# Optimization experiments

Measured on AMD Instinct MI355X. Metric: run time of the kernel, lower is better.

The kernel has to match this reference:

```python
import jax, jax.numpy as jnp
import numpy as np

HIDDEN_DIM = 128
ATTN_DIM = 64
B, N = 2, 512

def setup_inputs() -> dict:
    key = jax.random.key(0)
    ks = jax.random.split(key, 8)
    s = 0.05
    return {
        "X":    jax.random.normal(ks[0], (B, N, HIDDEN_DIM), dtype=jnp.float32),
        "Wo":   jax.random.normal(ks[1], (ATTN_DIM, HIDDEN_DIM), dtype=jnp.float32) * s,
        "W1":   jax.random.normal(ks[2], (ATTN_DIM, HIDDEN_DIM), dtype=jnp.float32) * s,
        "Wphi": jax.random.normal(ks[3], (ATTN_DIM,), dtype=jnp.float32) * s,
        "Wy":   jax.random.normal(ks[4], (HIDDEN_DIM, HIDDEN_DIM), dtype=jnp.float32) * s,
        "by":   jax.random.normal(ks[5], (HIDDEN_DIM,), dtype=jnp.float32) * s,
        "We":   jax.random.normal(ks[6], (HIDDEN_DIM, ATTN_DIM), dtype=jnp.float32) * s,
        "be":   jax.random.normal(ks[7], (HIDDEN_DIM,), dtype=jnp.float32) * s,
    }

def reference(X, Wo, W1, Wphi, Wy, by, We, be):
    # h_o, h_1: [B, N, A]
    h_o = jnp.einsum('bnc,ac->bna', X, Wo)
    h_1 = jnp.einsum('bnc,ac->bna', X, W1)
    # pairwise tanh edge features e_ij: [B, N, N, A]
    e = jnp.tanh(h_o[:, :, None, :] + h_1[:, None, :, :])
    # scores [B, N, N] via w_phi projection, row-wise softmax over j
    scores = jnp.einsum('bija,a->bij', e, Wphi)
    alpha = jax.nn.softmax(scores, axis=-1)
    # value path 1: Wy x_j -> aggregated by alpha (bmm)
    X_y = jnp.einsum('bnc,hc->bnh', X, Wy) + by
    part1 = jnp.einsum('bij,bjh->bih', alpha, X_y)
    # value path 2: We e_ij -> weighted sum over j
    eval_ = jnp.einsum('bija,ha->bijh', e, We) + be  # [B, N, N, H]
    part2 = jnp.einsum('bij,bijh->bih', alpha, eval_)
    return part1 + part2
```

## Files before the change

kernel.cpp:

```cpp
#include <hip/hip_runtime.h>

#define B_ 2
#define N_ 512
#define C_ 128
#define A_ 64
#define H_ 128
#define TI 2

#define SC2L 2.885390081777927f
#define NEG2LE -2.885390081777927f

#define OFF_WET 0
#define OFF_V   (OFF_WET + A_*H_)
#define OFF_US  (OFF_V  + B_*N_*A_)
#define OFF_UQ  (OFF_US + B_*N_*A_)
#define OFF_XY  (OFF_UQ + B_*N_*A_)

__device__ __forceinline__ float fexp2(float x) { return __builtin_amdgcn_exp2f(x); }
__device__ __forceinline__ float frcp(float x)  { return __builtin_amdgcn_rcpf(x); }

__global__ __launch_bounds__(512) void proj_kernel(
    const float* __restrict__ X, const float* __restrict__ Wo,
    const float* __restrict__ W1, const float* __restrict__ Wy,
    const float* __restrict__ by, const float* __restrict__ We,
    float* __restrict__ ws) {
  __shared__ float xs[2][C_];
  int row0 = blockIdx.x * 2;
  int t = threadIdx.x;
  if (t < 2*C_) xs[t >> 7][t & 127] = X[(size_t)row0*C_ + t];
  __syncthreads();

  int rsub = t >> 8;
  int col  = t & 255;
  int g = row0 + rsub;

  const float* W;
  if (col < 64)       W = Wo + (size_t)col*C_;
  else if (col < 128) W = W1 + (size_t)(col - 64)*C_;
  else                W = Wy + (size_t)(col - 128)*C_;

  const float4* w4 = (const float4*)W;
  const float4* x4 = (const float4*)xs[rsub];
  float acc = 0.f;
  #pragma unroll 8
  for (int k = 0; k < C_/4; ++k) {
    float4 wv = w4[k];
    float4 xv = x4[k];
    acc = fmaf(wv.x, xv.x, acc);
    acc = fmaf(wv.y, xv.y, acc);
    acc = fmaf(wv.z, xv.z, acc);
    acc = fmaf(wv.w, xv.w, acc);
  }

  if (col < 64) {
    ws[OFF_V + (size_t)g*A_ + col] = fexp2(SC2L * acc);
  } else if (col < 128) {
    int a = col - 64;
    float u = fexp2(SC2L * acc);
    ws[OFF_US + (size_t)g*A_ + a] = u;
    int b = g >> 9, n = g & (N_-1);
    ws[OFF_UQ + (((size_t)(b*16 + (a >> 2)))*N_ + n)*4 + (a & 3)] = u;
  } else {
    int h = col - 128;
    ws[OFF_XY + (size_t)g*H_ + h] = acc + by[h];
  }

  if (blockIdx.x == 0) {
    for (int k = t; k < A_*H_; k += 512) {
      int h = k >> 6, a = k & 63;
      ws[OFF_WET + a*H_ + h] = We[k];
    }
  }
}

__global__ __launch_bounds__(512) void attn_kernel(
    const float* __restrict__ Wphi, const float* __restrict__ be,
    const float* __restrict__ ws, float* __restrict__ out) {
  __shared__ float pkv0[A_], pkv1[A_], pkw[A_];
  __shared__ float sc[TI][N_];
  __shared__ float reds[TI][8];
  __shared__ float ebw[TI][8][A_];
  __shared__ float ebar[TI][A_];
  __shared__ float p1s[TI][4][H_];

  int t = threadIdx.x;
  int w = t >> 6, lane = t & 63;
  int blk = blockIdx.x;
  int b = blk >> 8;
  int i0 = (blk & 255) * TI;

  const float* vg  = ws + OFF_V  + (size_t)(b*N_ + i0)*A_;
  const float* us  = ws + OFF_US + (size_t)(b*N_)*A_;
  const float4* uq = (const float4*)(ws + OFF_UQ) + (size_t)b*16*N_;
  const float* xyg = ws + OFF_XY + (size_t)(b*N_)*H_;
  const float* wet = ws + OFF_WET;

  if (t < A_) {
    pkv0[t] = vg[t];
    pkv1[t] = vg[A_ + t];
    pkw[t]  = Wphi[t];
  }
  __syncthreads();

  float s0 = 0.f, s1 = 0.f;
  {
    #pragma unroll 4
    for (int a4 = 0; a4 < 16; ++a4) {
      float4 u  = uq[a4*N_ + t];
      float4 v0 = *(const float4*)&pkv0[a4*4];
      float4 v1 = *(const float4*)&pkv1[a4*4];
      float4 wq = *(const float4*)&pkw[a4*4];
      s0 = fmaf(wq.x, frcp(fmaf(v0.x, u.x, 1.f)), s0);
      s0 = fmaf(wq.y, frcp(fmaf(v0.y, u.y, 1.f)), s0);
      s0 = fmaf(wq.z, frcp(fmaf(v0.z, u.z, 1.f)), s0);
      s0 = fmaf(wq.w, frcp(fmaf(v0.w, u.w, 1.f)), s0);
      s1 = fmaf(wq.x, frcp(fmaf(v1.x, u.x, 1.f)), s1);
      s1 = fmaf(wq.y, frcp(fmaf(v1.y, u.y, 1.f)), s1);
      s1 = fmaf(wq.z, frcp(fmaf(v1.z, u.z, 1.f)), s1);
      s1 = fmaf(wq.w, frcp(fmaf(v1.w, u.w, 1.f)), s1);
    }
  }
  float p0 = fexp2(NEG2LE * s0), p1 = fexp2(NEG2LE * s1);
  float q0 = p0, q1 = p1;
  #pragma unroll
  for (int m = 1; m < 64; m <<= 1) { q0 += __shfl_xor(q0, m); q1 += __shfl_xor(q1, m); }
  sc[0][t] = p0; sc[1][t] = p1;
  if (lane == 0) { reds[0][w] = q0; reds[1][w] = q1; }
  __syncthreads();
  float l0 = reds[0][0], l1 = reds[1][0];
  #pragma unroll
  for (int k = 1; k < 8; ++k) { l0 += reds[0][k]; l1 += reds[1][k]; }

  {
    float v0 = pkv0[lane], v1 = pkv1[lane];
    float c0 = 0.f, c1 = 0.f;
    #pragma unroll 8
    for (int jj = 0; jj < N_/8; ++jj) {
      int j = jj*8 + w;
      float u = us[(size_t)j*A_ + lane];
      float pj0 = sc[0][j], pj1 = sc[1][j];
      c0 = fmaf(pj0, frcp(fmaf(v0, u, 1.f)), c0);
      c1 = fmaf(pj1, frcp(fmaf(v1, u, 1.f)), c1);
    }
    ebw[0][w][lane] = c0; ebw[1][w][lane] = c1;
  }

  {
    int h = t & 127, qd = t >> 7;
    const float* xq = xyg + (size_t)(qd*128)*H_ + h;
    float d0 = 0.f, d1 = 0.f;
    #pragma unroll 8
    for (int jc = 0; jc < 128; ++jc) {
      int j = qd*128 + jc;
      float xv = xq[(size_t)jc*H_];
      d0 = fmaf(sc[0][j], xv, d0);
      d1 = fmaf(sc[1][j], xv, d1);
    }
    p1s[0][qd][h] = d0; p1s[1][qd][h] = d1;
  }
  __syncthreads();

  if (t < TI*A_) {
    int r = t >> 6, a = t & 63;
    float e = 0.f;
    #pragma unroll
    for (int k = 0; k < 8; ++k) e += ebw[r][k][a];
    ebar[r][a] = (r ? l1 : l0) - 2.0f*e;
  }
  __syncthreads();

  if (t < TI*H_) {
    int h = t & 127, r = t >> 7;
    float acc = p1s[r][0][h] + p1s[r][1][h] + p1s[r][2][h] + p1s[r][3][h];
    float e2 = 0.f;
    #pragma unroll 8
    for (int a = 0; a < A_; ++a) e2 = fmaf(ebar[r][a], wet[a*H_ + h], e2);
    float l = r ? l1 : l0;
    out[(size_t)(b*N_ + i0 + r)*H_ + h] = (acc + e2) * frcp(l) + be[h];
  }
}

extern "C" void kernel_launch(void* const* d_in, const int* in_sizes, int n_in,
                              void* d_out, int out_size, void* d_ws, size_t ws_size,
                              hipStream_t stream) {
  const float* X    = (const float*)d_in[0];
  const float* Wo   = (const float*)d_in[1];
  const float* W1   = (const float*)d_in[2];
  const float* Wphi = (const float*)d_in[3];
  const float* Wy   = (const float*)d_in[4];
  const float* by   = (const float*)d_in[5];
  const float* We   = (const float*)d_in[6];
  const float* be   = (const float*)d_in[7];
  float* out = (float*)d_out;
  float* ws  = (float*)d_ws;

  hipLaunchKernelGGL(proj_kernel, dim3(B_*N_/2), dim3(512), 0, stream,
                     X, Wo, W1, Wy, by, We, ws);
  hipLaunchKernelGGL(attn_kernel, dim3(B_*N_/TI), dim3(512), 0, stream,
                     Wphi, be, ws, out);
}
```

Before: 108.5 us.

## Tile attention over j with shared-memory staged u and fewer threads

The attention kernel now walks the j dimension in tiles of 128 rows, staging the exp(h_1) values into LDS with a rotated (swizzled) layout. Both the score pass and the edge-sum pass read from this tile, so the separate transposed copy of u is no longer needed. The block shrinks to 256 threads with a 4-blocks-per-SM launch bound. Partial softmax sums, p-weighted edge sums and value sums are accumulated across tiles. This removes duplicate global reads and the extra workspace writes in proj_kernel, at the cost of more barriers per block and less parallelism per block.

```diff
diff --git a/kernel.cpp b/kernel.cpp
--- a/kernel.cpp
+++ b/kernel.cpp
@@ -6,6 +6,9 @@
 #define A_ 64
 #define H_ 128
 #define TI 2
+#define TJ 128
+#define NT (N_/TJ)
+#define THR 256
 
 #define SC2L 2.885390081777927f
 #define NEG2LE -2.885390081777927f
@@ -13,8 +16,7 @@
 #define OFF_WET 0
 #define OFF_V   (OFF_WET + A_*H_)
 #define OFF_US  (OFF_V  + B_*N_*A_)
-#define OFF_UQ  (OFF_US + B_*N_*A_)
-#define OFF_XY  (OFF_UQ + B_*N_*A_)
+#define OFF_XY  (OFF_US + B_*N_*A_)
 
 __device__ __forceinline__ float fexp2(float x) { return __builtin_amdgcn_exp2f(x); }
 __device__ __forceinline__ float frcp(float x)  { return __builtin_amdgcn_rcpf(x); }
@@ -55,14 +57,9 @@
   if (col < 64) {
     ws[OFF_V + (size_t)g*A_ + col] = fexp2(SC2L * acc);
   } else if (col < 128) {
-    int a = col - 64;
-    float u = fexp2(SC2L * acc);
-    ws[OFF_US + (size_t)g*A_ + a] = u;
-    int b = g >> 9, n = g & (N_-1);
-    ws[OFF_UQ + (((size_t)(b*16 + (a >> 2)))*N_ + n)*4 + (a & 3)] = u;
+    ws[OFF_US + (size_t)g*A_ + (col - 64)] = fexp2(SC2L * acc);
   } else {
-    int h = col - 128;
-    ws[OFF_XY + (size_t)g*H_ + h] = acc + by[h];
+    ws[OFF_XY + (size_t)g*H_ + (col - 128)] = acc + by[col - 128];
   }
 
   if (blockIdx.x == 0) {
@@ -73,15 +70,17 @@
   }
 }
 
-__global__ __launch_bounds__(512) void attn_kernel(
+__global__ __launch_bounds__(THR, 4) void attn_kernel(
     const float* __restrict__ Wphi, const float* __restrict__ be,
     const float* __restrict__ ws, float* __restrict__ out) {
-  __shared__ float pkv0[A_], pkv1[A_], pkw[A_];
-  __shared__ float sc[TI][N_];
-  __shared__ float reds[TI][8];
-  __shared__ float ebw[TI][8][A_];
+  __shared__ float4 u4[TJ][16];
+  __shared__ float sc[TI][TJ];
+  __shared__ __align__(16) float pkv[TI][A_];
+  __shared__ __align__(16) float pkw[A_];
+  __shared__ float ebw[TI][2][A_];
   __shared__ float ebar[TI][A_];
-  __shared__ float p1s[TI][4][H_];
+  __shared__ float p1s[TI][2][H_];
+  __shared__ float reds[TI][2];
 
   int t = threadIdx.x;
   int w = t >> 6, lane = t & 63;
@@ -89,93 +88,102 @@
   int b = blk >> 8;
   int i0 = (blk & 255) * TI;
 
-  const float* vg  = ws + OFF_V  + (size_t)(b*N_ + i0)*A_;
-  const float* us  = ws + OFF_US + (size_t)(b*N_)*A_;
-  const float4* uq = (const float4*)(ws + OFF_UQ) + (size_t)b*16*N_;
-  const float* xyg = ws + OFF_XY + (size_t)(b*N_)*H_;
-  const float* wet = ws + OFF_WET;
-
-  if (t < A_) {
-    pkv0[t] = vg[t];
-    pkv1[t] = vg[A_ + t];
-    pkw[t]  = Wphi[t];
-  }
-  __syncthreads();
-
-  float s0 = 0.f, s1 = 0.f;
-  {
-    #pragma unroll 4
-    for (int a4 = 0; a4 < 16; ++a4) {
-      float4 u  = uq[a4*N_ + t];
-      float4 v0 = *(const float4*)&pkv0[a4*4];
-      float4 v1 = *(const float4*)&pkv1[a4*4];
-      float4 wq = *(const float4*)&pkw[a4*4];
-      s0 = fmaf(wq.x, frcp(fmaf(v0.x, u.x, 1.f)), s0);
-      s0 = fmaf(wq.y, frcp(fmaf(v0.y, u.y, 1.f)), s0);
-      s0 = fmaf(wq.z, frcp(fmaf(v0.z, u.z, 1.f)), s0);
-      s0 = fmaf(wq.w, frcp(fmaf(v0.w, u.w, 1.f)), s0);
-      s1 = fmaf(wq.x, frcp(fmaf(v1.x, u.x, 1.f)), s1);
-      s1 = fmaf(wq.y, frcp(fmaf(v1.y, u.y, 1.f)), s1);
-      s1 = fmaf(wq.z, frcp(fmaf(v1.z, u.z, 1.f)), s1);
-      s1 = fmaf(wq.w, frcp(fmaf(v1.w, u.w, 1.f)), s1);
-    }
-  }
-  float p0 = fexp2(NEG2LE * s0), p1 = fexp2(NEG2LE * s1);
-  float q0 = p0, q1 = p1;
+  const float* vg   = ws + OFF_V + (size_t)(b*N_ + i0)*A_;
+  const float4* usb = (const float4*)(ws + OFF_US + (size_t)(b*N_)*A_);
+  const float* xyg  = ws + OFF_XY + (size_t)(b*N_)*H_;
+  const float* wet  = ws + OFF_WET;
+
+  if (t < TI*A_) { int r = t >> 6, a = t & 63; pkv[r][a] = vg[r*A_ + a]; }
+  if (t < A_)    pkw[t] = Wphi[t];
+  __syncthreads();
+
+  int rA = t >> 7, jA = t & 127;
+  int rC = w >> 1, wiC = w & 1;
+  int gp = t >> 7, hh = t & 127;
+
+  float vC = pkv[rC][lane];
+  float lacc = 0.f, cacc = 0.f, d0 = 0.f, d1 = 0.f;
+
+  for (int tile = 0; tile < NT; ++tile) {
+    int j0 = tile * TJ;
+    {
+      const float4* src = usb + (size_t)j0 * (A_/4);
+      #pragma unroll
+      for (int i = 0; i < (TJ*A_/4)/THR; ++i) {
+        int f = i*THR + t;
+        float4 val = src[f];
+        int jj = f >> 4, a4 = f & 15;
+        u4[jj][(a4 + jj) & 15] = val;
+      }
+    }
+    __syncthreads();
+
+    {
+      const float4* pv = (const float4*)&pkv[rA][0];
+      const float4* pw = (const float4*)&pkw[0];
+      float s = 0.f;
+      #pragma unroll 4
+      for (int a4 = 0; a4 < 16; ++a4) {
+        float4 u = u4[jA][(a4 + jA) & 15];
+        float4 v = pv[a4];
+        float4 wq = pw[a4];
+        s = fmaf(wq.x, frcp(fmaf(v.x, u.x, 1.f)), s);
+        s = fmaf(wq.y, frcp(fmaf(v.y, u.y, 1.f)), s);
+        s = fmaf(wq.z, frcp(fmaf(v.z, u.z, 1.f)), s);
+        s = fmaf(wq.w, frcp(fmaf(v.w, u.w, 1.f)), s);
+      }
+      float p = fexp2(NEG2LE * s);
+      sc[rA][jA] = p;
+      lacc += p;
+    }
+    __syncthreads();
+
+    {
+      #pragma unroll 4
+      for (int jj = 0; jj < TJ/2; ++jj) {
+        int j = jj*2 + wiC;
+        int q = ((lane >> 2) + j) & 15;
+        float u = ((const float*)&u4[j][q])[lane & 3];
+        float pj = sc[rC][j];
+        cacc = fmaf(pj, frcp(fmaf(vC, u, 1.f)), cacc);
+      }
+    }
+    {
+      const float* xq = xyg + (size_t)(j0 + gp*64)*H_ + hh;
+      #pragma unroll 4
+      for (int jc = 0; jc < 64; ++jc) {
+        int j = gp*64 + jc;
+        float xv = xq[(size_t)jc*H_];
+        d0 = fmaf(sc[0][j], xv, d0);
+        d1 = fmaf(sc[1][j], xv, d1);
+      }
+    }
+    __syncthreads();
+  }
+
+  ebw[rC][wiC][lane] = cacc;
+  p1s[0][gp][hh] = d0;
+  p1s[1][gp][hh] = d1;
   #pragma unroll
-  for (int m = 1; m < 64; m <<= 1) { q0 += __shfl_xor(q0, m); q1 += __shfl_xor(q1, m); }
-  sc[0][t] = p0; sc[1][t] = p1;
-  if (lane == 0) { reds[0][w] = q0; reds[1][w] = q1; }
-  __syncthreads();
-  float l0 = reds[0][0], l1 = reds[1][0];
-  #pragma unroll
-  for (int k = 1; k < 8; ++k) { l0 += reds[0][k]; l1 += reds[1][k]; }
-
-  {
-    float v0 = pkv0[lane], v1 = pkv1[lane];
-    float c0 = 0.f, c1 = 0.f;
-    #pragma unroll 8
-    for (int jj = 0; jj < N_/8; ++jj) {
-      int j = jj*8 + w;
-      float u = us[(size_t)j*A_ + lane];
-      float pj0 = sc[0][j], pj1 = sc[1][j];
-      c0 = fmaf(pj0, frcp(fmaf(v0, u, 1.f)), c0);
-      c1 = fmaf(pj1, frcp(fmaf(v1, u, 1.f)), c1);
-    }
-    ebw[0][w][lane] = c0; ebw[1][w][lane] = c1;
-  }
-
-  {
-    int h = t & 127, qd = t >> 7;
-    const float* xq = xyg + (size_t)(qd*128)*H_ + h;
-    float d0 = 0.f, d1 = 0.f;
-    #pragma unroll 8
-    for (int jc = 0; jc < 128; ++jc) {
-      int j = qd*128 + jc;
-      float xv = xq[(size_t)jc*H_];
-      d0 = fmaf(sc[0][j], xv, d0);
-      d1 = fmaf(sc[1][j], xv, d1);
-    }
-    p1s[0][qd][h] = d0; p1s[1][qd][h] = d1;
-  }
+  for (int m = 1; m < 64; m <<= 1) lacc += __shfl_xor(lacc, m);
+  if (lane == 0) reds[rA][w & 1] = lacc;
   __syncthreads();
 
   if (t < TI*A_) {
     int r = t >> 6, a = t & 63;
-    float e = 0.f;
-    #pragma unroll
-    for (int k = 0; k < 8; ++k) e += ebw[r][k][a];
-    ebar[r][a] = (r ? l1 : l0) - 2.0f*e;
-  }
-  __syncthreads();
-
-  if (t < TI*H_) {
-    int h = t & 127, r = t >> 7;
-    float acc = p1s[r][0][h] + p1s[r][1][h] + p1s[r][2][h] + p1s[r][3][h];
+    float e = ebw[r][0][a] + ebw[r][1][a];
+    float l = reds[r][0] + reds[r][1];
+    ebar[r][a] = l - 2.0f*e;
+  }
+  __syncthreads();
+
+  {
+    int r = t >> 7, h = t & 127;
+    float acc = p1s[r][0][h] + p1s[r][1][h];
     float e2 = 0.f;
     #pragma unroll 8
     for (int a = 0; a < A_; ++a) e2 = fmaf(ebar[r][a], wet[a*H_ + h], e2);
-    float l = r ? l1 : l0;
+    float l = reds[r][0] + reds[r][1];
     out[(size_t)(b*N_ + i0 + r)*H_ + h] = (acc + e2) * frcp(l) + be[h];
   }
 }
@@ -196,6 +204,6 @@
 
   hipLaunchKernelGGL(proj_kernel, dim3(B_*N_/2), dim3(512), 0, stream,
                      X, Wo, W1, Wy, by, We, ws);
-  hipLaunchKernelGGL(attn_kernel, dim3(B_*N_/TI), dim3(512), 0, stream,
+  hipLaunchKernelGGL(attn_kernel, dim3(B_*N_/TI), dim3(THR), 0, stream,
                      Wphi, be, ws, out);
 }
```

Result: slower. 124.0 us (+14.2%).
